# Optimization experiments

Measured on AMD Instinct MI355X. Metric: run time of the kernel, lower is better.

Reference implementation:

```python
import jax, jax.numpy as jnp
import numpy as np

B, T, S, PD = 512, 2048, 16, 4

def setup_inputs() -> dict:
    key = jax.random.key(0)
    ks = jax.random.split(key, 10)
    w = lambda k, sh: (jax.random.normal(k, sh, dtype=jnp.float32) * 0.1)
    return {
        'z': jax.random.normal(ks[0], (B, T, S), dtype=jnp.float32),
        'p': jax.random.normal(ks[1], (B, T, PD), dtype=jnp.float32),
        'mu0': jnp.zeros((B, S), dtype=jnp.float32),
        'P0': jnp.full((B, S), 0.1, dtype=jnp.float32),  # cfg['kf_P0']
        'Wq1': w(ks[2], (PD, 64)), 'bq1': jnp.zeros((64,), jnp.float32),
        'Wq2': w(ks[3], (64, S)),  'bq2': jnp.zeros((S,), jnp.float32),
        'Wr1': w(ks[4], (PD, 64)), 'br1': jnp.zeros((64,), jnp.float32),
        'Wr2': w(ks[5], (64, S)),  'br2': jnp.zeros((S,), jnp.float32),
        'Wg1': w(ks[6], (PD, 32)), 'bg1': jnp.zeros((32,), jnp.float32),
        'Wg2': w(ks[7], (32, 1)),  'bg2': jnp.zeros((1,), jnp.float32),
    }

def _mlp(x, W1, b1, W2, b2):
    return jax.nn.relu(x @ W1 + b1) @ W2 + b2

def reference(z, p, mu0, P0, Wq1, bq1, Wq2, bq2, Wr1, br1, Wr2, br2, Wg1, bg1, Wg2, bg2):
    # z: [B,T,S], p: [B,T,PD]; scan over time with batched Kalman state.
    zT = jnp.swapaxes(z, 0, 1)  # [T,B,S]
    pT = jnp.swapaxes(p, 0, 1)  # [T,B,PD]

    def step(carry, inp):
        mu, P = carry            # [B,S], [B,S]
        z_t, p_t = inp           # [B,S], [B,PD]
        Q_t = jax.nn.softplus(_mlp(p_t, Wq1, bq1, Wq2, bq2)) + 1e-8
        R_t = jax.nn.softplus(_mlp(p_t, Wr1, br1, Wr2, br2)) + 1e-8
        P_pred = P + Q_t
        K = jnp.clip(P_pred / (P_pred + R_t), 1e-6, 0.95)
        gamma_t = jax.nn.sigmoid(_mlp(p_t, Wg1, bg1, Wg2, bg2))  # [B,1] (scalar per sample)
        mu_new = mu + gamma_t * (K * (z_t - mu))
        P_new = (1.0 - K) * P_pred
        return (mu_new, P_new), mu_new

    (mu_f, P_f), mus = jax.lax.scan(step, (mu0, P0), (zT, pT))
    return jnp.swapaxes(mus, 0, 1)  # [B,T,S]
```

## Files before the change

### kernel.cpp

```cpp
#include <hip/hip_runtime.h>
#include <hip/hip_fp16.h>
#include <stdint.h>
#include <math.h>

#define KB 512
#define KT 2048
#define KS 16
#define KPD 4
#define QT 512
#define NQ (KT / QT)
#define HRS 168
#define QSTR 515

typedef _Float16 f16;
typedef _Float16 f16x8 __attribute__((ext_vector_type(8)));
typedef float f32x4 __attribute__((ext_vector_type(4)));

#define MFMA16(A, B, C) __builtin_amdgcn_mfma_f32_16x16x32_f16(A, B, C, 0, 0, 0)

__device__ __forceinline__ float softplus_f(float x) {
    float ax = fabsf(x);
    float e  = __expf(-ax);
    return fmaxf(x, 0.0f) + __logf(1.0f + e);
}
__device__ __forceinline__ float sigmoid_f(float x) {
    return __builtin_amdgcn_rcpf(1.0f + __expf(-x));
}
__device__ __forceinline__ float h2f_lo(uint32_t w) {
    return __half2float(__ushort_as_half((unsigned short)(w & 0xffffu)));
}
__device__ __forceinline__ float h2f_hi(uint32_t w) {
    return __half2float(__ushort_as_half((unsigned short)(w >> 16)));
}
__device__ __forceinline__ f16x8 zero8() {
    f16x8 v;
#pragma unroll
    for (int i = 0; i < 8; ++i) v[i] = (f16)0;
    return v;
}
__device__ __forceinline__ int spos(int t) { return t ^ ((t >> 5) & 31); }

__global__ __launch_bounds__(512, 2) void kalman_one(
    const float* __restrict__ z, const float* __restrict__ p,
    const float* __restrict__ mu0, const float* __restrict__ P0,
    const float* __restrict__ Wq1, const float* __restrict__ bq1,
    const float* __restrict__ Wq2, const float* __restrict__ bq2,
    const float* __restrict__ Wr1, const float* __restrict__ br1,
    const float* __restrict__ Wr2, const float* __restrict__ br2,
    const float* __restrict__ Wg1, const float* __restrict__ bg1,
    const float* __restrict__ Wg2, const float* __restrict__ bg2,
    float* __restrict__ out)
{
    __shared__ __align__(16) uint32_t QRl[KS * QSTR];
    __shared__ __align__(16) float    Gl[QT];
    __shared__ __align__(16) uint32_t Ubuf[10752];

    const int tid = threadIdx.x;
    const int wv = tid >> 6;
    const int l = tid & 63;
    const int g = l >> 4;
    const int c = l & 15;
    const int b = blockIdx.x;

    f16* __restrict__ Hw = reinterpret_cast<f16*>(Ubuf) + wv * (KS * HRS);
    float* __restrict__ zs = reinterpret_cast<float*>(Ubuf);

    const float* __restrict__ zb = z + (size_t)b * KT * KS;
    const float* __restrict__ pb = p + (size_t)b * KT * KPD;
    float* __restrict__ ob = out + (size_t)b * KT * KS;

    f16x8 fA1[10];
#pragma unroll
    for (int m = 0; m < 10; ++m) {
        const float* W = (m < 4) ? (Wq1 + m * 16)
                       : (m < 8) ? (Wr1 + (m - 4) * 16)
                                 : (Wg1 + (m - 8) * 16);
        const int ld = (m < 8) ? 64 : 32;
        float w0 = W[0 * ld + c], w1 = W[1 * ld + c],
              w2 = W[2 * ld + c], w3 = W[3 * ld + c];
        f16x8 a = zero8();
        if (g == 0) { a[0] = (f16)w0; a[1] = (f16)w1; a[2] = (f16)w2; a[3] = (f16)w3; }
        fA1[m] = a;
    }
    f16x8 fA2[5];
#pragma unroll
    for (int i = 0; i < 4; ++i) {
        const float* W = (i < 2) ? Wq2 : Wr2;
        const int kb = (i & 1) * 32;
        f16x8 a;
#pragma unroll
        for (int j = 0; j < 8; ++j) a[j] = (f16)W[(kb + g * 8 + j) * 16 + c];
        fA2[i] = a;
    }
    {
        f16x8 a = zero8();
        if (c == 0) {
#pragma unroll
            for (int j = 0; j < 8; ++j) a[j] = (f16)Wg2[g * 8 + j];
        }
        fA2[4] = a;
    }
    const float bQ0 = bq2[g * 4 + 0], bQ1 = bq2[g * 4 + 1],
                bQ2 = bq2[g * 4 + 2], bQ3 = bq2[g * 4 + 3];
    const float bR0 = br2[g * 4 + 0], bR1 = br2[g * 4 + 1],
                bR2 = br2[g * 4 + 2], bR3 = br2[g * 4 + 3];
    const float bG = bg2[0];

    float muA = mu0[b * KS + wv],     PA = P0[b * KS + wv];
    float muB = mu0[b * KS + wv + 8], PB = P0[b * KS + wv + 8];

    auto scan_s = [&](int s, float& mu_q, float& P_q) {
        uint32_t qr[8];
        const uint32_t* qrow = QRl + (size_t)s * QSTR;
        float zvv[8], gvv[8];
#pragma unroll
        for (int i = 0; i < 8; ++i) {
            const int ps = spos(l * 8 + i);
            qr[i] = qrow[ps];
            zvv[i] = zs[s * QSTR + ps];
            gvv[i] = Gl[ps];
        }
        float c00 = 1.f, c01 = 0.f, c10 = 0.f, c11 = 1.f;
#pragma unroll
        for (int i = 0; i < 8; ++i) {
            float Q = h2f_lo(qr[i]), R = h2f_hi(qr[i]);
            float ta = fmaf(Q, c10, c00);
            float tb = fmaf(Q, c11, c01);
            float n10 = fmaf(Q + R, c10, c00);
            float n11 = fmaf(Q + R, c11, c01);
            c00 = R * ta; c01 = R * tb; c10 = n10; c11 = n11;
        }
        float rn = __builtin_amdgcn_rcpf(c11);
        float ma = c00 * rn, mb = c01 * rn, mc = c10 * rn;
#pragma unroll
        for (int r = 0; r < 6; ++r) {
            const int d = 1 << r;
            float pa = __shfl_up(ma, d);
            float pbv = __shfl_up(mb, d);
            float pc = __shfl_up(mc, d);
            float na = fmaf(ma, pa, mb * pc);
            float nb = fmaf(ma, pbv, mb);
            float nc = fmaf(mc, pa, pc);
            float nd = fmaf(mc, pbv, 1.f);
            float rr = __builtin_amdgcn_rcpf(nd);
            bool act = (l >= d);
            ma = act ? na * rr : ma;
            mb = act ? nb * rr : mb;
            mc = act ? nc * rr : mc;
        }
        float ea = __shfl_up(ma, 1);
        float eb = __shfl_up(mb, 1);
        float ec = __shfl_up(mc, 1);
        if (l == 0) { ea = 1.f; eb = 0.f; ec = 0.f; }
        float P = fmaf(ea, P_q, eb) * __builtin_amdgcn_rcpf(fmaf(ec, P_q, 1.f));

        float av[8], bw[8];
        float A = 1.f, Bv = 0.f;
#pragma unroll
        for (int i = 0; i < 8; ++i) {
            float Q = h2f_lo(qr[i]), R = h2f_hi(qr[i]);
            float Pp = P + Q;
            float K0 = Pp * __builtin_amdgcn_rcpf(Pp + R);
            float Kk = __builtin_amdgcn_fmed3f(K0, 1e-6f, 0.95f);
            float gk = gvv[i] * Kk;
            av[i] = 1.f - gk;
            bw[i] = gk * zvv[i];
            P = fmaf(-Kk, Pp, Pp);
            A = A * av[i];
            Bv = fmaf(av[i], Bv, bw[i]);
        }
        float P_end = __shfl(P, 63);
#pragma unroll
        for (int r = 0; r < 6; ++r) {
            const int d = 1 << r;
            float pA = __shfl_up(A, d);
            float pB = __shfl_up(Bv, d);
            float nA = A * pA;
            float nB = fmaf(A, pB, Bv);
            bool act = (l >= d);
            A  = act ? nA : A;
            Bv = act ? nB : Bv;
        }
        float eA = __shfl_up(A, 1);
        float eB = __shfl_up(Bv, 1);
        if (l == 0) { eA = 1.f; eB = 0.f; }
        float mu = fmaf(eA, mu_q, eB);
#pragma unroll
        for (int i = 0; i < 8; ++i) {
            mu = fmaf(av[i], mu, bw[i]);
            zs[s * QSTR + spos(l * 8 + i)] = mu;
        }
        mu_q = __shfl(mu, 63);
        P_q = P_end;
    };

    for (int q = 0; q < NQ; ++q) {
        {
            const int trow = q * QT + wv * 64;
            const float4 pv = *reinterpret_cast<const float4*>(pb + (size_t)(trow + l) * KPD);

            f16x8 fBP[4];
#pragma unroll
            for (int n = 0; n < 4; ++n) {
                const int src = n * 16 + c;
                float x = __shfl(pv.x, src);
                float y = __shfl(pv.y, src);
                float zz = __shfl(pv.z, src);
                float w = __shfl(pv.w, src);
                f16x8 v = zero8();
                if (g == 0) { v[0] = (f16)x; v[1] = (f16)y; v[2] = (f16)zz; v[3] = (f16)w; }
                fBP[n] = v;
            }

#pragma unroll
            for (int n = 0; n < 4; ++n) {
#pragma unroll
                for (int m = 0; m < 10; ++m) {
                    const float* bs = (m < 4) ? (bq1 + m * 16)
                                    : (m < 8) ? (br1 + (m - 4) * 16)
                                              : (bg1 + (m - 8) * 16);
                    f32x4 acc;
                    acc[0] = bs[g * 4 + 0]; acc[1] = bs[g * 4 + 1];
                    acc[2] = bs[g * 4 + 2]; acc[3] = bs[g * 4 + 3];
                    acc = MFMA16(fA1[m], fBP[n], acc);
                    auto h01 = __builtin_amdgcn_cvt_pkrtz(fmaxf(acc[0], 0.f), fmaxf(acc[1], 0.f));
                    auto h23 = __builtin_amdgcn_cvt_pkrtz(fmaxf(acc[2], 0.f), fmaxf(acc[3], 0.f));
                    uint32_t w0, w1;
                    __builtin_memcpy(&w0, &h01, 4);
                    __builtin_memcpy(&w1, &h23, 4);
                    *reinterpret_cast<uint32_t*>(&Hw[c * HRS + m * 16 + g * 4 + 0]) = w0;
                    *reinterpret_cast<uint32_t*>(&Hw[c * HRS + m * 16 + g * 4 + 2]) = w1;
                }
                f16x8 fb0 = *reinterpret_cast<const f16x8*>(&Hw[c * HRS + 0 * 32 + g * 8]);
                f16x8 fb1 = *reinterpret_cast<const f16x8*>(&Hw[c * HRS + 1 * 32 + g * 8]);
                f16x8 fb2 = *reinterpret_cast<const f16x8*>(&Hw[c * HRS + 2 * 32 + g * 8]);
                f16x8 fb3 = *reinterpret_cast<const f16x8*>(&Hw[c * HRS + 3 * 32 + g * 8]);
                f16x8 fb4 = *reinterpret_cast<const f16x8*>(&Hw[c * HRS + 4 * 32 + g * 8]);

                f32x4 aq; aq[0] = bQ0; aq[1] = bQ1; aq[2] = bQ2; aq[3] = bQ3;
                aq = MFMA16(fA2[0], fb0, aq);
                aq = MFMA16(fA2[1], fb1, aq);
                f32x4 ar; ar[0] = bR0; ar[1] = bR1; ar[2] = bR2; ar[3] = bR3;
                ar = MFMA16(fA2[2], fb2, ar);
                ar = MFMA16(fA2[3], fb3, ar);
                f32x4 ag; ag[0] = 0.f; ag[1] = 0.f; ag[2] = 0.f; ag[3] = 0.f;
                ag = MFMA16(fA2[4], fb4, ag);

                const int tt = wv * 64 + n * 16 + c;
                const int ps = spos(tt);
#pragma unroll
                for (int i = 0; i < 4; ++i) {
                    float Qv = softplus_f(aq[i]) + 1e-8f;
                    float Rv = softplus_f(ar[i]) + 1e-8f;
                    auto pk = __builtin_amdgcn_cvt_pkrtz(Qv, Rv);
                    uint32_t w; __builtin_memcpy(&w, &pk, 4);
                    QRl[(size_t)(g * 4 + i) * QSTR + ps] = w;
                }
                if (g == 0)
                    Gl[ps] = sigmoid_f(ag[0] + bG);
            }
        }
        __syncthreads();

        {
            const float4* zq = reinterpret_cast<const float4*>(zb + (size_t)q * QT * KS);
#pragma unroll
            for (int v = 0; v < 4; ++v) {
                int k = tid + 512 * v;
                float4 w = zq[k];
                int t = k >> 2, s0 = (k & 3) << 2;
                const int ps = spos(t);
                zs[(s0 + 0) * QSTR + ps] = w.x;
                zs[(s0 + 1) * QSTR + ps] = w.y;
                zs[(s0 + 2) * QSTR + ps] = w.z;
                zs[(s0 + 3) * QSTR + ps] = w.w;
            }
        }
        __syncthreads();

        scan_s(wv, muA, PA);
        scan_s(wv + 8, muB, PB);
        __syncthreads();

        {
            float* od = ob + (size_t)q * QT * KS;
#pragma unroll
            for (int v = 0; v < 4; ++v) {
                int k = tid + 512 * v;
                int t = k >> 2, s0 = (k & 3) << 2;
                const int ps = spos(t);
                float4 w;
                w.x = zs[(s0 + 0) * QSTR + ps];
                w.y = zs[(s0 + 1) * QSTR + ps];
                w.z = zs[(s0 + 2) * QSTR + ps];
                w.w = zs[(s0 + 3) * QSTR + ps];
                *reinterpret_cast<float4*>(od + 4 * (size_t)k) = w;
            }
        }
        __syncthreads();
    }
}

extern "C" void kernel_launch(void* const* d_in, const int* in_sizes, int n_in,
                              void* d_out, int out_size, void* d_ws, size_t ws_size,
                              hipStream_t stream) {
    const float* z   = (const float*)d_in[0];
    const float* p   = (const float*)d_in[1];
    const float* mu0 = (const float*)d_in[2];
    const float* P0  = (const float*)d_in[3];
    const float* Wq1 = (const float*)d_in[4];
    const float* bq1 = (const float*)d_in[5];
    const float* Wq2 = (const float*)d_in[6];
    const float* bq2 = (const float*)d_in[7];
    const float* Wr1 = (const float*)d_in[8];
    const float* br1 = (const float*)d_in[9];
    const float* Wr2 = (const float*)d_in[10];
    const float* br2 = (const float*)d_in[11];
    const float* Wg1 = (const float*)d_in[12];
    const float* bg1 = (const float*)d_in[13];
    const float* Wg2 = (const float*)d_in[14];
    const float* bg2 = (const float*)d_in[15];
    float* out = (float*)d_out;

    hipLaunchKernelGGL(kalman_one, dim3(KB), dim3(512), 0, stream,
                       z, p, mu0, P0, Wq1, bq1, Wq2, bq2,
                       Wr1, br1, Wr2, br2, Wg1, bg1, Wg2, bg2, out);
}
```

Before: 86.58 us.

## Transpose MLP hidden layer via lane shuffles instead of LDS staging

```diff
diff --git a/kernel.cpp b/kernel.cpp
--- a/kernel.cpp
+++ b/kernel.cpp
@@ -9,7 +9,6 @@
 #define KPD 4
 #define QT 512
 #define NQ (KT / QT)
-#define HRS 168
 #define QSTR 515
 
 typedef _Float16 f16;
@@ -40,7 +39,13 @@
 }
 __device__ __forceinline__ int spos(int t) { return t ^ ((t >> 5) & 31); }
 
-__global__ __launch_bounds__(512, 2) void kalman_one(
+__device__ __forceinline__ uint32_t pkrelu(float a, float b) {
+    auto h = __builtin_amdgcn_cvt_pkrtz(fmaxf(a, 0.f), fmaxf(b, 0.f));
+    uint32_t w; __builtin_memcpy(&w, &h, 4);
+    return w;
+}
+
+__global__ __launch_bounds__(512, 4) void kalman_one(
     const float* __restrict__ z, const float* __restrict__ p,
     const float* __restrict__ mu0, const float* __restrict__ P0,
     const float* __restrict__ Wq1, const float* __restrict__ bq1,
@@ -53,7 +58,7 @@
 {
     __shared__ __align__(16) uint32_t QRl[KS * QSTR];
     __shared__ __align__(16) float    Gl[QT];
-    __shared__ __align__(16) uint32_t Ubuf[10752];
+    __shared__ __align__(16) float    zs[KS * QSTR];
 
     const int tid = threadIdx.x;
     const int wv = tid >> 6;
@@ -61,9 +66,6 @@
     const int g = l >> 4;
     const int c = l & 15;
     const int b = blockIdx.x;
-
-    f16* __restrict__ Hw = reinterpret_cast<f16*>(Ubuf) + wv * (KS * HRS);
-    float* __restrict__ zs = reinterpret_cast<float*>(Ubuf);
 
     const float* __restrict__ zb = z + (size_t)b * KT * KS;
     const float* __restrict__ pb = p + (size_t)b * KT * KPD;
@@ -106,6 +108,10 @@
                 bR2 = br2[g * 4 + 2], bR3 = br2[g * 4 + 3];
     const float bG = bg2[0];
 
+    const int sa = ((g & 1) * 2) * 16 + c;
+    const int sb = sa + 16;
+    const bool hiM = (g >= 2);
+
     float muA = mu0[b * KS + wv],     PA = P0[b * KS + wv];
     float muB = mu0[b * KS + wv + 8], PB = P0[b * KS + wv + 8];
 
@@ -123,12 +129,12 @@
         float c00 = 1.f, c01 = 0.f, c10 = 0.f, c11 = 1.f;
 #pragma unroll
         for (int i = 0; i < 8; ++i) {
-            float Q = h2f_lo(qr[i]), R = h2f_hi(qr[i]);
+            float Q = h2f_lo(qr[i]), Rr = h2f_hi(qr[i]);
             float ta = fmaf(Q, c10, c00);
             float tb = fmaf(Q, c11, c01);
-            float n10 = fmaf(Q + R, c10, c00);
-            float n11 = fmaf(Q + R, c11, c01);
-            c00 = R * ta; c01 = R * tb; c10 = n10; c11 = n11;
+            float n10 = fmaf(Q + Rr, c10, c00);
+            float n11 = fmaf(Q + Rr, c11, c01);
+            c00 = Rr * ta; c01 = Rr * tb; c10 = n10; c11 = n11;
         }
         float rn = __builtin_amdgcn_rcpf(c11);
         float ma = c00 * rn, mb = c01 * rn, mc = c10 * rn;
@@ -158,9 +164,9 @@
         float A = 1.f, Bv = 0.f;
 #pragma unroll
         for (int i = 0; i < 8; ++i) {
-            float Q = h2f_lo(qr[i]), R = h2f_hi(qr[i]);
+            float Q = h2f_lo(qr[i]), Rr = h2f_hi(qr[i]);
             float Pp = P + Q;
-            float K0 = Pp * __builtin_amdgcn_rcpf(Pp + R);
+            float K0 = Pp * __builtin_amdgcn_rcpf(Pp + Rr);
             float Kk = __builtin_amdgcn_fmed3f(K0, 1e-6f, 0.95f);
             float gk = gvv[i] * Kk;
             av[i] = 1.f - gk;
@@ -199,52 +205,68 @@
             const int trow = q * QT + wv * 64;
             const float4 pv = *reinterpret_cast<const float4*>(pb + (size_t)(trow + l) * KPD);
 
-            f16x8 fBP[4];
 #pragma unroll
             for (int n = 0; n < 4; ++n) {
-                const int src = n * 16 + c;
-                float x = __shfl(pv.x, src);
-                float y = __shfl(pv.y, src);
-                float zz = __shfl(pv.z, src);
-                float w = __shfl(pv.w, src);
-                f16x8 v = zero8();
-                if (g == 0) { v[0] = (f16)x; v[1] = (f16)y; v[2] = (f16)zz; v[3] = (f16)w; }
-                fBP[n] = v;
-            }
-
-#pragma unroll
-            for (int n = 0; n < 4; ++n) {
-#pragma unroll
-                for (int m = 0; m < 10; ++m) {
-                    const float* bs = (m < 4) ? (bq1 + m * 16)
-                                    : (m < 8) ? (br1 + (m - 4) * 16)
-                                              : (bg1 + (m - 8) * 16);
-                    f32x4 acc;
-                    acc[0] = bs[g * 4 + 0]; acc[1] = bs[g * 4 + 1];
-                    acc[2] = bs[g * 4 + 2]; acc[3] = bs[g * 4 + 3];
-                    acc = MFMA16(fA1[m], fBP[n], acc);
-                    auto h01 = __builtin_amdgcn_cvt_pkrtz(fmaxf(acc[0], 0.f), fmaxf(acc[1], 0.f));
-                    auto h23 = __builtin_amdgcn_cvt_pkrtz(fmaxf(acc[2], 0.f), fmaxf(acc[3], 0.f));
-                    uint32_t w0, w1;
-                    __builtin_memcpy(&w0, &h01, 4);
-                    __builtin_memcpy(&w1, &h23, 4);
-                    *reinterpret_cast<uint32_t*>(&Hw[c * HRS + m * 16 + g * 4 + 0]) = w0;
-                    *reinterpret_cast<uint32_t*>(&Hw[c * HRS + m * 16 + g * 4 + 2]) = w1;
+                f16x8 fBP;
+                {
+                    const int src = n * 16 + c;
+                    float x = __shfl(pv.x, src);
+                    float y = __shfl(pv.y, src);
+                    float zz = __shfl(pv.z, src);
+                    float w = __shfl(pv.w, src);
+                    fBP = zero8();
+                    if (g == 0) { fBP[0] = (f16)x; fBP[1] = (f16)y; fBP[2] = (f16)zz; fBP[3] = (f16)w; }
                 }
-                f16x8 fb0 = *reinterpret_cast<const f16x8*>(&Hw[c * HRS + 0 * 32 + g * 8]);
-                f16x8 fb1 = *reinterpret_cast<const f16x8*>(&Hw[c * HRS + 1 * 32 + g * 8]);
-                f16x8 fb2 = *reinterpret_cast<const f16x8*>(&Hw[c * HRS + 2 * 32 + g * 8]);
-                f16x8 fb3 = *reinterpret_cast<const f16x8*>(&Hw[c * HRS + 3 * 32 + g * 8]);
-                f16x8 fb4 = *reinterpret_cast<const f16x8*>(&Hw[c * HRS + 4 * 32 + g * 8]);
 
                 f32x4 aq; aq[0] = bQ0; aq[1] = bQ1; aq[2] = bQ2; aq[3] = bQ3;
-                aq = MFMA16(fA2[0], fb0, aq);
-                aq = MFMA16(fA2[1], fb1, aq);
                 f32x4 ar; ar[0] = bR0; ar[1] = bR1; ar[2] = bR2; ar[3] = bR3;
-                ar = MFMA16(fA2[2], fb2, ar);
-                ar = MFMA16(fA2[3], fb3, ar);
                 f32x4 ag; ag[0] = 0.f; ag[1] = 0.f; ag[2] = 0.f; ag[3] = 0.f;
-                ag = MFMA16(fA2[4], fb4, ag);
+
+#pragma unroll
+                for (int X = 0; X < 5; ++X) {
+                    const int m0 = 2 * X, m1 = 2 * X + 1;
+                    uint32_t a0, a1, b0, b1;
+                    {
+                        const float* bs = (m0 < 4) ? (bq1 + m0 * 16)
+                                        : (m0 < 8) ? (br1 + (m0 - 4) * 16)
+                                                   : (bg1 + (m0 - 8) * 16);
+                        f32x4 acc;
+                        acc[0] = bs[g * 4 + 0]; acc[1] = bs[g * 4 + 1];
+                        acc[2] = bs[g * 4 + 2]; acc[3] = bs[g * 4 + 3];
+                        acc = MFMA16(fA1[m0], fBP, acc);
+                        a0 = pkrelu(acc[0], acc[1]);
+                        a1 = pkrelu(acc[2], acc[3]);
+                    }
+                    {
+                        const float* bs = (m1 < 4) ? (bq1 + m1 * 16)
+                                        : (m1 < 8) ? (br1 + (m1 - 4) * 16)
+                                                   : (bg1 + (m1 - 8) * 16);
+                        f32x4 acc;
+                        acc[0] = bs[g * 4 + 0]; acc[1] = bs[g * 4 + 1];
+                        acc[2] = bs[g * 4 + 2]; acc[3] = bs[g * 4 + 3];
+                        acc = MFMA16(fA1[m1], fBP, acc);
+                        b0 = pkrelu(acc[0], acc[1]);
+                        b1 = pkrelu(acc[2], acc[3]);
+                    }
+                    uint32_t t0 = __shfl(a0, sa), t1 = __shfl(a1, sa);
+                    uint32_t t2 = __shfl(a0, sb), t3 = __shfl(a1, sb);
+                    uint32_t u0 = __shfl(b0, sa), u1 = __shfl(b1, sa);
+                    uint32_t u2 = __shfl(b0, sb), u3 = __shfl(b1, sb);
+                    uint32_t w0 = hiM ? u0 : t0;
+                    uint32_t w1 = hiM ? u1 : t1;
+                    uint32_t w2 = hiM ? u2 : t2;
+                    uint32_t w3 = hiM ? u3 : t3;
+                    f16x8 fb;
+                    __builtin_memcpy(&fb, &w0, 4);
+                    __builtin_memcpy(reinterpret_cast<char*>(&fb) + 4, &w1, 4);
+                    __builtin_memcpy(reinterpret_cast<char*>(&fb) + 8, &w2, 4);
+                    __builtin_memcpy(reinterpret_cast<char*>(&fb) + 12, &w3, 4);
+                    if (X == 0)      aq = MFMA16(fA2[0], fb, aq);
+                    else if (X == 1) aq = MFMA16(fA2[1], fb, aq);
+                    else if (X == 2) ar = MFMA16(fA2[2], fb, ar);
+                    else if (X == 3) ar = MFMA16(fA2[3], fb, ar);
+                    else             ag = MFMA16(fA2[4], fb, ag);
+                }
 
                 const int tt = wv * 64 + n * 16 + c;
                 const int ps = spos(tt);
@@ -259,10 +281,7 @@
                 if (g == 0)
                     Gl[ps] = sigmoid_f(ag[0] + bG);
             }
-        }
-        __syncthreads();
-
-        {
+
             const float4* zq = reinterpret_cast<const float4*>(zb + (size_t)q * QT * KS);
 #pragma unroll
             for (int v = 0; v < 4; ++v) {
```

After: 201.8 us. 133% more time.
